# Kernel optimization log

Hardware: AMD Instinct MI355X
Metric: run time of the kernel (lower is better)

The kernel has to match this reference:

```python
import jax, jax.numpy as jnp
import numpy as np
from math import sqrt

NKEY = 64


def setup_inputs() -> dict:
    key = jax.random.key(0)
    ks = jax.random.split(key, 8)
    B, Nfield, Nquery, Nkey, Nval, Lf, Lq = 4, 128, 128, 64, 64, 4096, 4096
    field = jax.random.normal(ks[0], (B, Nfield, Lf), dtype=jnp.float32)
    query = jax.random.normal(ks[1], (B, Nquery, Lq), dtype=jnp.float32)
    # conv1d(kernel=1) weights as [out_ch, in_ch] matrices + bias
    scale_f = 1.0 / sqrt(Nfield)
    scale_q = 1.0 / sqrt(Nquery)
    W_fk = jax.random.normal(ks[2], (Nkey, Nfield), dtype=jnp.float32) * scale_f
    b_fk = jax.random.normal(ks[3], (Nkey,), dtype=jnp.float32) * scale_f
    W_fv = jax.random.normal(ks[4], (Nval, Nfield), dtype=jnp.float32) * scale_f
    b_fv = jax.random.normal(ks[5], (Nval,), dtype=jnp.float32) * scale_f
    W_qk = jax.random.normal(ks[6], (Nkey, Nquery), dtype=jnp.float32) * scale_q
    b_qk = jax.random.normal(ks[7], (Nkey,), dtype=jnp.float32) * scale_q
    return {"field": field, "query": query, "W_fk": W_fk, "b_fk": b_fk,
            "W_fv": W_fv, "b_fv": b_fv, "W_qk": W_qk, "b_qk": b_qk}


def reference(field, query, W_fk, b_fk, W_fv, b_fv, W_qk, b_qk):
    # 1x1-conv projections == per-position linear over channel dim
    fkeys = jnp.einsum('kf,bfl->bkl', W_fk, field) + b_fk[None, :, None]   # [B,Nkey,Lf]
    fvals = jnp.einsum('vf,bfl->bvl', W_fv, field) + b_fv[None, :, None]   # [B,Nval,Lf]
    hkeys = jnp.einsum('kq,bql->bkl', W_qk, query) + b_qk[None, :, None]   # [B,Nkey,Lq]
    # scores: [B, Lf, Lq]
    z = jnp.einsum('bkl,bkq->blq', fkeys, hkeys) / sqrt(NKEY)
    w = jnp.exp(jnp.clip(z, -30.0, 30.0))
    w = w / (jnp.sum(w, axis=1, keepdims=True) + 1e-16)  # normalize over field length
    y = jnp.einsum('bvl,blq->bvq', fvals, w)             # [B,Nval,Lq]
    return y
```

## Files before the change

kernel.cpp:

```cpp
#include <hip/hip_runtime.h>
#include <hip/hip_bf16.h>

typedef unsigned short u16;
typedef __bf16 bf16x8 __attribute__((ext_vector_type(8)));
typedef __bf16 bf16x4 __attribute__((ext_vector_type(4)));
typedef float f32x4 __attribute__((ext_vector_type(4)));
typedef unsigned int uint32x2 __attribute__((ext_vector_type(2)));

#define MFMA16(a, b, c) __builtin_amdgcn_mfma_f32_16x16x32_bf16(a, b, c, 0, 0, 0)

#define FK_SCALE 0.1803368801111204f

#define NSPLIT 8

__global__ __launch_bounds__(64, 2) void proj_kernel(
    const float* __restrict__ field, const float* __restrict__ query,
    const float* __restrict__ Wfk, const float* __restrict__ bfk,
    const float* __restrict__ Wfv, const float* __restrict__ bfv,
    const float* __restrict__ Wqk, const float* __restrict__ bqk,
    u16* __restrict__ fkF, u16* __restrict__ fvF, u16* __restrict__ hkF) {
  const int lane = threadIdx.x;
  const int q15 = lane & 15, quad = lane >> 4;
  const int bx = blockIdx.x;
  const int p = bx >> 8;
  const int b = (bx >> 6) & 3;
  const int l0 = (bx & 63) * 64;

  const float* src  = (p == 2) ? query : field;
  const float* W    = (p == 0) ? Wfk : (p == 1) ? Wfv : Wqk;
  const float* bias = (p == 0) ? bfk : (p == 1) ? bfv : bqk;
  const float* sp = src + (size_t)b * (128 * 4096);

  bf16x8 fr1[4][4];
#pragma unroll
  for (int t = 0; t < 4; ++t)
#pragma unroll
    for (int ks = 0; ks < 4; ++ks) {
      const float* pp = sp + (size_t)(ks * 32 + quad * 8) * 4096 + l0 + t * 16 + q15;
      bf16x8 v;
#pragma unroll
      for (int j = 0; j < 8; ++j) v[j] = (__bf16)pp[(size_t)j * 4096];
      fr1[t][ks] = v;
    }

  bf16x8 fr2[4][4];
#pragma unroll
  for (int t = 0; t < 4; ++t)
#pragma unroll
    for (int ks = 0; ks < 4; ++ks) {
      const float* pp = W + (size_t)(t * 16 + q15) * 128 + ks * 32 + quad * 8;
      f32x4 w0 = *reinterpret_cast<const f32x4*>(pp);
      f32x4 w1 = *reinterpret_cast<const f32x4*>(pp + 4);
      bf16x8 v;
#pragma unroll
      for (int j = 0; j < 4; ++j) { v[j] = (__bf16)w0[j]; v[4 + j] = (__bf16)w1[j]; }
      fr2[t][ks] = v;
    }

#pragma unroll
  for (int nn = 0; nn < 4; ++nn) {
    f32x4 Cn[4];
#pragma unroll
    for (int mm = 0; mm < 4; ++mm) Cn[mm] = (f32x4){0.f, 0.f, 0.f, 0.f};
#pragma unroll
    for (int ks = 0; ks < 4; ++ks)
#pragma unroll
      for (int mm = 0; mm < 4; ++mm)
        Cn[mm] = (p == 1) ? MFMA16(fr1[mm][ks], fr2[nn][ks], Cn[mm])
                          : MFMA16(fr2[mm][ks], fr1[nn][ks], Cn[mm]);

    if (p == 1) {
      const float bv = bias[nn * 16 + q15];
#pragma unroll
      for (int mm = 0; mm < 4; ++mm) {
        bf16x4 o;
#pragma unroll
        for (int r = 0; r < 4; ++r) o[r] = (__bf16)(Cn[mm][r] + bv);
        u16* dst = fvF +
            ((size_t)((b * 4 + nn) * 64 + (l0 >> 6)) * 2 + (mm >> 1)) * 512 +
            (((2 * mm + (quad >> 1)) & 3) * 16 + q15) * 8 + (quad & 1) * 4;
        *reinterpret_cast<uint32x2*>(dst) = __builtin_bit_cast(uint32x2, o);
      }
    } else {
      const float cs = (p == 0) ? FK_SCALE : 1.0f;
      u16* outF = (p == 0) ? fkF : hkF;
#pragma unroll
      for (int mm = 0; mm < 4; ++mm) {
        f32x4 bz = *reinterpret_cast<const f32x4*>(bias + mm * 16 + quad * 4);
        bf16x4 o;
#pragma unroll
        for (int r = 0; r < 4; ++r) o[r] = (__bf16)((Cn[mm][r] + bz[r]) * cs);
        u16* dst = outF +
            ((size_t)((b * 256 + (l0 >> 4) + nn) * 2) + (mm >> 1)) * 512 +
            (((2 * mm + (quad >> 1)) & 3) * 16 + q15) * 8 + (quad & 1) * 4;
        *reinterpret_cast<uint32x2*>(dst) = __builtin_bit_cast(uint32x2, o);
      }
    }
  }
}

__global__ __launch_bounds__(64, 2) void attn_kernel(
    const u16* __restrict__ fkF, const u16* __restrict__ hkF,
    const u16* __restrict__ fvF, float* __restrict__ Ynum,
    float* __restrict__ den) {
  constexpr int LL = 4096, CH = 64, NITER = (LL / NSPLIT) / CH;
  const int lane = threadIdx.x;
  const int q15 = lane & 15;
  const int quad = lane >> 4;
  const int id = blockIdx.x;
  const int b = id & 3;
  const int qblk = (id >> 2) & 63;
  const int split = id >> 8;
  const int l0base = split * (LL / NSPLIT);

  __shared__ __align__(16) char sP[2][8192];

  bf16x8 hkf[4][2];
#pragma unroll
  for (int j = 0; j < 4; ++j)
#pragma unroll
    for (int ks = 0; ks < 2; ++ks)
      hkf[j][ks] = *reinterpret_cast<const bf16x8*>(
          hkF + ((size_t)((b * 256 + qblk * 4 + j) * 2 + ks)) * 512 + lane * 8);

  bf16x8 ones;
#pragma unroll
  for (int j = 0; j < 8; ++j) ones[j] = (__bf16)1.0f;

  f32x4 Yacc[4][4];
#pragma unroll
  for (int mm = 0; mm < 4; ++mm)
#pragma unroll
    for (int nn = 0; nn < 4; ++nn) Yacc[mm][nn] = (f32x4){0.f, 0.f, 0.f, 0.f};
  f32x4 denAcc[4];
#pragma unroll
  for (int nn = 0; nn < 4; ++nn) denAcc[nn] = (f32x4){0.f, 0.f, 0.f, 0.f};

  const int wbase = (quad >> 1) * 256 + q15 * 16 + (quad & 1) * 8;
  const int rbase = lane * 16;

  bf16x8 fkf[4][2];
  bf16x8 af[4][2];

  auto loadFK = [&](int l0) {
    const int t0 = l0 >> 4;
#pragma unroll
    for (int s = 0; s < 4; ++s)
#pragma unroll
      for (int ks = 0; ks < 2; ++ks)
        fkf[s][ks] = *reinterpret_cast<const bf16x8*>(
            fkF + ((size_t)((b * 256 + t0 + s) * 2 + ks)) * 512 + lane * 8);
  };
  auto loadAF = [&](int l0) {
    const int cl = l0 >> 6;
#pragma unroll
    for (int mm = 0; mm < 4; ++mm)
#pragma unroll
      for (int ks = 0; ks < 2; ++ks)
        af[mm][ks] = *reinterpret_cast<const bf16x8*>(
            fvF + ((size_t)(((b * 4 + mm) * 64 + cl) * 2 + ks)) * 512 + lane * 8);
  };
  auto Sphase = [&](char* sPb) {
#pragma unroll
    for (int s = 0; s < 4; ++s) {
      f32x4 accS[4];
#pragma unroll
      for (int jj = 0; jj < 4; ++jj) accS[jj] = (f32x4){0.f, 0.f, 0.f, 0.f};
#pragma unroll
      for (int ks = 0; ks < 2; ++ks)
#pragma unroll
        for (int jj = 0; jj < 4; ++jj)
          accS[jj] = MFMA16(fkf[s][ks], hkf[jj][ks], accS[jj]);
      char* wp = sPb + (s >> 1) * 4096 + (s & 1) * 512 + wbase;
#pragma unroll
      for (int jj = 0; jj < 4; ++jj) {
        bf16x4 pk;
#pragma unroll
        for (int r = 0; r < 4; ++r)
          pk[r] = (__bf16)__builtin_amdgcn_exp2f(accS[jj][r]);
        *reinterpret_cast<uint32x2*>(wp + jj * 1024) =
            __builtin_bit_cast(uint32x2, pk);
      }
    }
  };
  auto PVphase = [&](const char* sPr) {
#pragma unroll
    for (int ks = 0; ks < 2; ++ks) {
      bf16x8 bfr[4];
#pragma unroll
      for (int nn = 0; nn < 4; ++nn)
        bfr[nn] = *reinterpret_cast<const bf16x8*>(
            sPr + ks * 4096 + nn * 1024 + rbase);
#pragma unroll
      for (int nn = 0; nn < 4; ++nn)
        denAcc[nn] = MFMA16(ones, bfr[nn], denAcc[nn]);
#pragma unroll
      for (int mm = 0; mm < 4; ++mm)
#pragma unroll
        for (int nn = 0; nn < 4; ++nn)
          Yacc[mm][nn] = MFMA16(af[mm][ks], bfr[nn], Yacc[mm][nn]);
    }
  };

  loadFK(l0base);
  loadAF(l0base);
  Sphase(sP[0]);
  loadFK(l0base + CH);

#pragma unroll 2
  for (int it = 1; it < NITER; ++it) {
    const int l0 = l0base + it * CH;
    Sphase(sP[it & 1]);
    if (it + 1 < NITER) loadFK(l0 + CH);
    PVphase(sP[(it - 1) & 1]);
    loadAF(l0);
  }
  PVphase(sP[(NITER - 1) & 1]);

  const size_t slot = ((size_t)split * 4 + b) * 64 + qblk;
  if (quad == 0) {
#pragma unroll
    for (int nn = 0; nn < 4; ++nn)
      den[slot * 64 + nn * 16 + q15] = denAcc[nn][0];
  }
  float* Yo = Ynum + slot * 4096;
#pragma unroll
  for (int mm = 0; mm < 4; ++mm)
#pragma unroll
    for (int nn = 0; nn < 4; ++nn)
      *reinterpret_cast<f32x4*>(Yo + (mm * 4 + nn) * 256 + lane * 4) =
          Yacc[mm][nn];
}

__global__ __launch_bounds__(256) void combine_kernel(
    const float* __restrict__ Yn, const float* __restrict__ dn,
    float* __restrict__ out) {
  const int idx = blockIdx.x * 256 + threadIdx.x;
  const int q = idx & 4095;
  const int v = (idx >> 12) & 63;
  const int b = idx >> 18;
  const int qb = q >> 6;
  const int mm = v >> 4, md = (v >> 2) & 3, r = v & 3;
  const int nn = (q >> 4) & 3, lane = md * 16 + (q & 15);
  float num = 0.f, d = 1e-16f;
#pragma unroll
  for (int s = 0; s < NSPLIT; ++s) {
    const size_t slot = ((size_t)s * 4 + b) * 64 + qb;
    num += Yn[slot * 4096 + (mm * 4 + nn) * 256 + lane * 4 + r];
    d += dn[slot * 64 + (q & 63)];
  }
  out[idx] = num / d;
}

extern "C" void kernel_launch(void* const* d_in, const int* in_sizes, int n_in,
                              void* d_out, int out_size, void* d_ws,
                              size_t ws_size, hipStream_t stream) {
  const float* field = (const float*)d_in[0];
  const float* query = (const float*)d_in[1];
  const float* Wfk = (const float*)d_in[2];
  const float* bfk = (const float*)d_in[3];
  const float* Wfv = (const float*)d_in[4];
  const float* bfv = (const float*)d_in[5];
  const float* Wqk = (const float*)d_in[6];
  const float* bqk = (const float*)d_in[7];
  float* out = (float*)d_out;

  char* ws = (char*)d_ws;
  u16* fkF = (u16*)(ws);
  u16* hkF = (u16*)(ws + (2ull << 20));
  u16* fvF = (u16*)(ws + (4ull << 20));
  float* Ynum = (float*)(ws + (6ull << 20));
  float* den = (float*)(ws + (38ull << 20));

  proj_kernel<<<dim3(768), 64, 0, stream>>>(field, query, Wfk, bfk, Wfv, bfv,
                                            Wqk, bqk, fkF, fvF, hkF);
  attn_kernel<<<dim3(2048), 64, 0, stream>>>(fkF, hkF, fvF, Ynum, den);
  combine_kernel<<<dim3(4096), 256, 0, stream>>>(Ynum, den, out);
}
```

Measured before the change: 117.9 us.

## Double split count, single-buffer LDS, VALU denominator, bf16 partial outputs

```diff
diff --git a/kernel.cpp b/kernel.cpp
--- a/kernel.cpp
+++ b/kernel.cpp
@@ -11,7 +11,7 @@
 
 #define FK_SCALE 0.1803368801111204f
 
-#define NSPLIT 8
+#define NSPLIT 16
 
 __global__ __launch_bounds__(64, 2) void proj_kernel(
     const float* __restrict__ field, const float* __restrict__ query,
@@ -99,9 +99,9 @@
   }
 }
 
-__global__ __launch_bounds__(64, 2) void attn_kernel(
+__global__ __launch_bounds__(64, 3) void attn_kernel(
     const u16* __restrict__ fkF, const u16* __restrict__ hkF,
-    const u16* __restrict__ fvF, float* __restrict__ Ynum,
+    const u16* __restrict__ fvF, u16* __restrict__ Ynum,
     float* __restrict__ den) {
   constexpr int LL = 4096, CH = 64, NITER = (LL / NSPLIT) / CH;
   const int lane = threadIdx.x;
@@ -113,7 +113,7 @@
   const int split = id >> 8;
   const int l0base = split * (LL / NSPLIT);
 
-  __shared__ __align__(16) char sP[2][8192];
+  __shared__ __align__(16) char sP[8192];
 
   bf16x8 hkf[4][2];
 #pragma unroll
@@ -123,18 +123,12 @@
       hkf[j][ks] = *reinterpret_cast<const bf16x8*>(
           hkF + ((size_t)((b * 256 + qblk * 4 + j) * 2 + ks)) * 512 + lane * 8);
 
-  bf16x8 ones;
-#pragma unroll
-  for (int j = 0; j < 8; ++j) ones[j] = (__bf16)1.0f;
-
   f32x4 Yacc[4][4];
 #pragma unroll
   for (int mm = 0; mm < 4; ++mm)
 #pragma unroll
     for (int nn = 0; nn < 4; ++nn) Yacc[mm][nn] = (f32x4){0.f, 0.f, 0.f, 0.f};
-  f32x4 denAcc[4];
-#pragma unroll
-  for (int nn = 0; nn < 4; ++nn) denAcc[nn] = (f32x4){0.f, 0.f, 0.f, 0.f};
+  float dsum[4] = {0.f, 0.f, 0.f, 0.f};
 
   const int wbase = (quad >> 1) * 256 + q15 * 16 + (quad & 1) * 8;
   const int rbase = lane * 16;
@@ -160,7 +154,7 @@
         af[mm][ks] = *reinterpret_cast<const bf16x8*>(
             fvF + ((size_t)(((b * 4 + mm) * 64 + cl) * 2 + ks)) * 512 + lane * 8);
   };
-  auto Sphase = [&](char* sPb) {
+  auto Sphase = [&]() {
 #pragma unroll
     for (int s = 0; s < 4; ++s) {
       f32x4 accS[4];
@@ -171,29 +165,31 @@
 #pragma unroll
         for (int jj = 0; jj < 4; ++jj)
           accS[jj] = MFMA16(fkf[s][ks], hkf[jj][ks], accS[jj]);
-      char* wp = sPb + (s >> 1) * 4096 + (s & 1) * 512 + wbase;
+      char* wp = sP + (s >> 1) * 4096 + (s & 1) * 512 + wbase;
 #pragma unroll
       for (int jj = 0; jj < 4; ++jj) {
         bf16x4 pk;
-#pragma unroll
-        for (int r = 0; r < 4; ++r)
-          pk[r] = (__bf16)__builtin_amdgcn_exp2f(accS[jj][r]);
+        float ds = 0.f;
+#pragma unroll
+        for (int r = 0; r < 4; ++r) {
+          float e = __builtin_amdgcn_exp2f(accS[jj][r]);
+          pk[r] = (__bf16)e;
+          ds += e;
+        }
+        dsum[jj] += ds;
         *reinterpret_cast<uint32x2*>(wp + jj * 1024) =
             __builtin_bit_cast(uint32x2, pk);
       }
     }
   };
-  auto PVphase = [&](const char* sPr) {
+  auto PVphase = [&]() {
 #pragma unroll
     for (int ks = 0; ks < 2; ++ks) {
       bf16x8 bfr[4];
 #pragma unroll
       for (int nn = 0; nn < 4; ++nn)
         bfr[nn] = *reinterpret_cast<const bf16x8*>(
-            sPr + ks * 4096 + nn * 1024 + rbase);
-#pragma unroll
-      for (int nn = 0; nn < 4; ++nn)
-        denAcc[nn] = MFMA16(ones, bfr[nn], denAcc[nn]);
+            sP + ks * 4096 + nn * 1024 + rbase);
 #pragma unroll
       for (int mm = 0; mm < 4; ++mm)
 #pragma unroll
@@ -204,36 +200,41 @@
 
   loadFK(l0base);
   loadAF(l0base);
-  Sphase(sP[0]);
+  Sphase();
   loadFK(l0base + CH);
 
-#pragma unroll 2
+#pragma unroll
   for (int it = 1; it < NITER; ++it) {
-    const int l0 = l0base + it * CH;
-    Sphase(sP[it & 1]);
-    if (it + 1 < NITER) loadFK(l0 + CH);
-    PVphase(sP[(it - 1) & 1]);
-    loadAF(l0);
-  }
-  PVphase(sP[(NITER - 1) & 1]);
+    PVphase();
+    Sphase();
+    loadAF(l0base + it * CH);
+    if (it + 1 < NITER) loadFK(l0base + (it + 1) * CH);
+  }
+  PVphase();
 
   const size_t slot = ((size_t)split * 4 + b) * 64 + qblk;
-  if (quad == 0) {
-#pragma unroll
-    for (int nn = 0; nn < 4; ++nn)
-      den[slot * 64 + nn * 16 + q15] = denAcc[nn][0];
-  }
-  float* Yo = Ynum + slot * 4096;
+#pragma unroll
+  for (int jj = 0; jj < 4; ++jj) {
+    float d = dsum[jj];
+    d += __shfl_xor(d, 16, 64);
+    d += __shfl_xor(d, 32, 64);
+    if (quad == 0) den[slot * 64 + jj * 16 + q15] = d;
+  }
+  u16* Yo = Ynum + slot * 4096;
 #pragma unroll
   for (int mm = 0; mm < 4; ++mm)
 #pragma unroll
-    for (int nn = 0; nn < 4; ++nn)
-      *reinterpret_cast<f32x4*>(Yo + (mm * 4 + nn) * 256 + lane * 4) =
-          Yacc[mm][nn];
+    for (int nn = 0; nn < 4; ++nn) {
+      bf16x4 o;
+#pragma unroll
+      for (int r = 0; r < 4; ++r) o[r] = (__bf16)Yacc[mm][nn][r];
+      *reinterpret_cast<uint32x2*>(Yo + (mm * 4 + nn) * 256 + lane * 4) =
+          __builtin_bit_cast(uint32x2, o);
+    }
 }
 
 __global__ __launch_bounds__(256) void combine_kernel(
-    const float* __restrict__ Yn, const float* __restrict__ dn,
+    const u16* __restrict__ Yn, const float* __restrict__ dn,
     float* __restrict__ out) {
   const int idx = blockIdx.x * 256 + threadIdx.x;
   const int q = idx & 4095;
@@ -242,11 +243,12 @@
   const int qb = q >> 6;
   const int mm = v >> 4, md = (v >> 2) & 3, r = v & 3;
   const int nn = (q >> 4) & 3, lane = md * 16 + (q & 15);
+  const int off = (mm * 4 + nn) * 256 + lane * 4 + r;
   float num = 0.f, d = 1e-16f;
 #pragma unroll
   for (int s = 0; s < NSPLIT; ++s) {
     const size_t slot = ((size_t)s * 4 + b) * 64 + qb;
-    num += Yn[slot * 4096 + (mm * 4 + nn) * 256 + lane * 4 + r];
+    num += (float)__builtin_bit_cast(__bf16, Yn[slot * 4096 + off]);
     d += dn[slot * 64 + (q & 63)];
   }
   out[idx] = num / d;
@@ -269,11 +271,11 @@
   u16* fkF = (u16*)(ws);
   u16* hkF = (u16*)(ws + (2ull << 20));
   u16* fvF = (u16*)(ws + (4ull << 20));
-  float* Ynum = (float*)(ws + (6ull << 20));
+  u16* Ynum = (u16*)(ws + (6ull << 20));
   float* den = (float*)(ws + (38ull << 20));
 
   proj_kernel<<<dim3(768), 64, 0, stream>>>(field, query, Wfk, bfk, Wfv, bfv,
                                             Wqk, bqk, fkF, fvF, hkF);
-  attn_kernel<<<dim3(2048), 64, 0, stream>>>(fkF, hkF, fvF, Ynum, den);
+  attn_kernel<<<dim3(4096), 64, 0, stream>>>(fkF, hkF, fvF, Ynum, den);
   combine_kernel<<<dim3(4096), 256, 0, stream>>>(Ynum, den, out);
 }
```

After: 288.4 us. 2.45x slower.
